# Kernel tuning notes

Measured on AMD Instinct MI355X. Metric: run time of the kernel, lower is better.

Reference implementation:

```python
import jax, jax.numpy as jnp
import numpy as np

B, S, D = 1, 4096, 2048
H, KVH, HD = 16, 4, 128  # heads, kv heads, head_dim
ROPE_BASE = 10000.0


def _rope_cos_sin(position_ids):
    # inv_freq: [HD/2]
    inv_freq = 1.0 / (ROPE_BASE ** (jnp.arange(0, HD, 2, dtype=jnp.float32) / HD))
    # freqs: [B, S, HD/2] -> emb: [B, S, HD] (concat(freqs, freqs))
    freqs = position_ids.astype(jnp.float32)[..., None] * inv_freq
    emb = jnp.concatenate([freqs, freqs], axis=-1)
    # [B, 1, S, HD] to broadcast over heads
    return jnp.cos(emb)[:, None, :, :], jnp.sin(emb)[:, None, :, :]


def _rotate_half(x):
    x1, x2 = x[..., : HD // 2], x[..., HD // 2 :]
    return jnp.concatenate([-x2, x1], axis=-1)


def setup_inputs() -> dict:
    key = jax.random.key(0)
    ks = jax.random.split(key, 5)
    s = 0.02
    return {
        "hidden_states": jax.random.normal(ks[0], (B, S, D), jnp.float32),
        "Wq": jax.random.normal(ks[1], (H * HD, D), jnp.float32) * s,
        "Wk": jax.random.normal(ks[2], (KVH * HD, D), jnp.float32) * s,
        "Wv": jax.random.normal(ks[3], (KVH * HD, D), jnp.float32) * s,
        "Wo": jax.random.normal(ks[4], (D, H * HD), jnp.float32) * s,
        "position_ids": jnp.arange(S, dtype=jnp.int64 if jax.config.jax_enable_x64 else jnp.int32)[None, :].repeat(B, 0),
    }


def reference(hidden_states, Wq, Wk, Wv, Wo, position_ids):
    b, s, _ = hidden_states.shape
    # projections (no bias): [b, s, nheads*hd] -> [b, nh, s, hd]
    q = (hidden_states @ Wq.T).reshape(b, s, H, HD).transpose(0, 2, 1, 3)
    k = (hidden_states @ Wk.T).reshape(b, s, KVH, HD).transpose(0, 2, 1, 3)
    v = (hidden_states @ Wv.T).reshape(b, s, KVH, HD).transpose(0, 2, 1, 3)

    cos, sin = _rope_cos_sin(position_ids)  # [b,1,s,hd]
    q = q * cos + _rotate_half(q) * sin
    k = k * cos + _rotate_half(k) * sin

    # GQA: repeat kv heads (repeat_interleave along head dim)
    n_rep = H // KVH
    k = jnp.repeat(k, n_rep, axis=1)
    v = jnp.repeat(v, n_rep, axis=1)

    # eager quadratic attention with causal mask
    scores = jnp.einsum("bhqd,bhkd->bhqk", q, k) / jnp.sqrt(jnp.float32(HD))
    causal = jnp.tril(jnp.ones((s, s), dtype=bool))
    scores = jnp.where(causal[None, None], scores, jnp.finfo(scores.dtype).min)
    attn = jax.nn.softmax(scores, axis=-1)
    out = jnp.einsum("bhqk,bhkd->bhqd", attn, v)  # [b,h,s,hd]
    out = out.transpose(0, 2, 1, 3).reshape(b, s, H * HD)
    return out @ Wo.T
```

## Files before the change

### kernel.cpp

```cpp
#include <hip/hip_runtime.h>
#include <hip/hip_bf16.h>

constexpr int S   = 4096;
constexpr int D   = 2048;
constexpr int H   = 16;
constexpr int KVH = 4;
constexpr int HD  = 128;

using short8 = __attribute__((ext_vector_type(8))) short;
using f32x4  = __attribute__((ext_vector_type(4))) float;
using f32x16 = __attribute__((ext_vector_type(16))) float;

__device__ inline ushort f2bf(float f) {
  union { float f; unsigned u; } x{f};
  unsigned r = x.u + 0x7FFFu + ((x.u >> 16) & 1u);
  return (ushort)(r >> 16);
}
__device__ inline float bf2f(ushort h) {
  union { unsigned u; float f; } x{(unsigned)h << 16};
  return x.f;
}
__device__ inline unsigned pkbf(float a, float b) {
  union { float f; unsigned u; } xa{a}, xb{b};
  unsigned ra = xa.u + 0x7FFFu + ((xa.u >> 16) & 1u);
  unsigned rb = xb.u + 0x7FFFu + ((xb.u >> 16) & 1u);
#if __has_builtin(__builtin_amdgcn_perm)
  return __builtin_amdgcn_perm(rb, ra, 0x07060302u);
#else
  return (rb & 0xFFFF0000u) | (ra >> 16);
#endif
}
__device__ inline unsigned pkbf_t(float a, float b) {
  union { float f; unsigned u; } xa{a}, xb{b};
#if __has_builtin(__builtin_amdgcn_perm)
  return __builtin_amdgcn_perm(xb.u, xa.u, 0x07060302u);
#else
  return (xb.u & 0xFFFF0000u) | (xa.u >> 16);
#endif
}
__device__ inline float fast_exp2(float x) {
#if __has_builtin(__builtin_amdgcn_exp2f)
  return __builtin_amdgcn_exp2f(x);
#else
  return exp2f(x);
#endif
}

__device__ inline void async_copy16(const ushort* g, ushort* l) {
  __builtin_amdgcn_global_load_lds(
      (const __attribute__((address_space(1))) unsigned int*)g,
      (__attribute__((address_space(3))) unsigned int*)l, 16, 0, 0);
}

constexpr size_t N_HID = (size_t)S * D;
constexpr size_t N_WQ  = (size_t)(H * HD) * D;
constexpr size_t N_WKV = (size_t)(KVH * HD) * D;
constexpr size_t C1_ = N_HID;
constexpr size_t C2_ = C1_ + N_WQ;
constexpr size_t C3_ = C2_ + N_WKV;
constexpr size_t C4_ = C3_ + N_WKV;
constexpr size_t C5_ = C4_ + N_WQ;

__global__ void cvt_all_kernel(const float* __restrict__ hid, const float* __restrict__ wq,
                               const float* __restrict__ wk, const float* __restrict__ wv,
                               const float* __restrict__ wo, ushort* __restrict__ dst) {
  size_t i = (size_t)blockIdx.x * blockDim.x + threadIdx.x;
  size_t off = i * 4;
  if (off >= C5_) return;
  const float* src;
  if      (off < C1_) src = hid + off;
  else if (off < C2_) src = wq + (off - C1_);
  else if (off < C3_) src = wk + (off - C2_);
  else if (off < C4_) src = wv + (off - C3_);
  else                src = wo + (off - C4_);
  float4 f = *(const float4*)src;
  ushort4 o;
  o.x = f2bf(f.x); o.y = f2bf(f.y); o.z = f2bf(f.z); o.w = f2bf(f.w);
  *(ushort4*)&dst[off] = o;
}

template <int OUT_MODE>
__device__ __forceinline__ void gemm_tile(const ushort* __restrict__ A,
                                          const ushort* __restrict__ Bt,
                                          void* __restrict__ Cv,
                                          int M, int N, int K, int bxi, int byi,
                                          ushort* As, ushort* Bs) {
  const int bm = byi * 128;
  const int bn = bxi * 128;
  const int tid  = threadIdx.x;
  const int lane = tid & 63;
  const int w    = tid >> 6;
  const int wr = w >> 1, wc = w & 1;
  const int lm = lane & 15, quad = lane >> 4;

  f32x4 acc[4][4];
#pragma unroll
  for (int i = 0; i < 4; ++i)
#pragma unroll
    for (int j = 0; j < 4; ++j) acc[i][j] = (f32x4){0.f, 0.f, 0.f, 0.f};

  for (int k0 = 0; k0 < K; k0 += 32) {
#pragma unroll
    for (int j = 0; j < 2; ++j) {
      int idx = j * 256 + tid;
      int row = idx >> 2;
      int col = (idx & 3) * 8;
      int ubase = (j * 256 + w * 64) * 8;
      async_copy16(A + (size_t)(bm + row) * K + k0 + col, &As[ubase]);
      async_copy16(Bt + (size_t)(bn + row) * K + k0 + col, &Bs[ubase]);
    }
    __syncthreads();
    short8 af[4], bfr[4];
#pragma unroll
    for (int t = 0; t < 4; ++t) {
      af[t]  = *(const short8*)&As[(wr * 64 + t * 16 + lm) * 32 + quad * 8];
      bfr[t] = *(const short8*)&Bs[(wc * 64 + t * 16 + lm) * 32 + quad * 8];
    }
#pragma unroll
    for (int i = 0; i < 4; ++i)
#pragma unroll
      for (int j = 0; j < 4; ++j)
        acc[i][j] = __builtin_amdgcn_mfma_f32_16x16x32_bf16(af[i], bfr[j], acc[i][j], 0, 0, 0);
    __syncthreads();
  }

#pragma unroll
  for (int i = 0; i < 4; ++i)
#pragma unroll
    for (int j = 0; j < 4; ++j) {
      if (OUT_MODE == 2) {
        int col  = bn + wc * 64 + j * 16 + lm;
        int rowb = bm + wr * 64 + i * 16 + quad * 4;
        ushort4 o4;
        o4.x = f2bf(acc[i][j][0]); o4.y = f2bf(acc[i][j][1]);
        o4.z = f2bf(acc[i][j][2]); o4.w = f2bf(acc[i][j][3]);
        *(ushort4*)&((ushort*)Cv)[(size_t)col * M + rowb] = o4;
      } else {
#pragma unroll
        for (int r = 0; r < 4; ++r) {
          size_t row = bm + wr * 64 + i * 16 + quad * 4 + r;
          size_t col = bn + wc * 64 + j * 16 + lm;
          if (OUT_MODE == 1) ((ushort*)Cv)[row * N + col] = f2bf(acc[i][j][r]);
          else               ((float*)Cv)[row * N + col]  = acc[i][j][r];
        }
      }
    }
}

__global__ __launch_bounds__(256) void gemm_qkv_kernel(const ushort* __restrict__ hb,
                                                       const ushort* __restrict__ wq,
                                                       const ushort* __restrict__ wk,
                                                       const ushort* __restrict__ wv,
                                                       ushort* __restrict__ qb,
                                                       ushort* __restrict__ kb,
                                                       ushort* __restrict__ vtb) {
  __shared__ __align__(16) ushort As[128 * 32];
  __shared__ __align__(16) ushort Bs[128 * 32];
  int bid = blockIdx.x;
  if (bid < 512) {
    gemm_tile<1>(hb, wq, qb, S, H * HD, D, bid & 15, bid >> 4, As, Bs);
  } else if (bid < 640) {
    int b = bid - 512;
    gemm_tile<1>(hb, wk, kb, S, KVH * HD, D, b & 3, b >> 2, As, Bs);
  } else {
    int b = bid - 640;
    gemm_tile<2>(hb, wv, vtb, S, KVH * HD, D, b & 3, b >> 2, As, Bs);
  }
}

template <int OUT_MODE>
__global__ __launch_bounds__(256) void gemm_bt_kernel(const ushort* __restrict__ A,
                                                      const ushort* __restrict__ Bt,
                                                      void* __restrict__ Cv,
                                                      int M, int N, int K) {
  __shared__ __align__(16) ushort As[128 * 32];
  __shared__ __align__(16) ushort Bs[128 * 32];
  gemm_tile<OUT_MODE>(A, Bt, Cv, M, N, K, blockIdx.x, blockIdx.y, As, Bs);
}

__global__ void rope_bf16_kernel(ushort* __restrict__ qb, ushort* __restrict__ kb,
                                 const int* __restrict__ pos_ids) {
  int idx = blockIdx.x * blockDim.x + threadIdx.x;
  const int total = S * (H + KVH) * (HD / 2);
  if (idx >= total) return;
  int j = idx & 63;
  int t = idx >> 6;
  int head = t % (H + KVH);
  int s = t / (H + KVH);
  float p = (float)pos_ids[s];
  float inv_freq = exp2f(-(float)j * (13.287712379549449f / 64.0f));
  float ang = p * inv_freq;
  float c = cosf(ang), sn = sinf(ang);
  ushort* base = (head < H) ? (qb + (size_t)s * (H * HD) + head * HD)
                            : (kb + (size_t)s * (KVH * HD) + (head - H) * HD);
  float x1 = bf2f(base[j]), x2 = bf2f(base[j + 64]);
  base[j]      = f2bf(x1 * c - x2 * sn);
  base[j + 64] = f2bf(x2 * c + x1 * sn);
}

__global__ __launch_bounds__(256, 2) void attn_mfma_kernel(const ushort* __restrict__ q,
                                                           const ushort* __restrict__ k,
                                                           const ushort* __restrict__ Vt,
                                                           ushort* __restrict__ o) {
  const int bid = blockIdx.x;
  const int h   = bid & 15;
  const int t   = bid >> 4;
  const int tl  = t & 15, hi = t >> 4;
  const int qi  = hi ? (2 * tl) : (31 - 2 * tl);
  const int q0  = qi * 128;
  const int kvh = h >> 2;
  const int tid  = threadIdx.x;
  const int lane = tid & 63;
  const int w    = tid >> 6;
  const int m32  = lane & 31;
  const int p    = lane >> 5;

  __shared__ __align__(16) ushort Kc[2][8192];
  __shared__ __align__(16) ushort Vs[2][8192];

  const int q0w = q0 + w * 32;

  short8 qf[8];
#pragma unroll
  for (int s = 0; s < 8; ++s)
    qf[s] = *(const short8*)&q[(size_t)(q0w + m32) * (H * HD) + h * HD + s * 16 + p * 8];

  f32x16 Oacc[4];
#pragma unroll
  for (int i = 0; i < 4; ++i)
#pragma unroll
    for (int r = 0; r < 16; ++r) Oacc[i][r] = 0.f;
  float lsum = 0.f;

  auto stage = [&](int k0, int buf) {
#pragma unroll
    for (int i = 0; i < 8; ++i) {
      int c = w * 8 + i;
      if (c < 16) {
        int kh = c >> 3, s = c & 7;
        async_copy16(&k[(size_t)(k0 + kh * 32 + m32) * (KVH * HD) + kvh * HD + s * 16 + p * 8],
                     &Kc[buf][c * 512]);
      } else {
        int cv = c - 16;
        int ht = cv >> 2, t2 = cv & 3;
        async_copy16(&Vt[(size_t)(kvh * HD + ht * 32 + m32) * S + k0 + t2 * 16 + p * 8],
                     &Vs[buf][cv * 512]);
      }
    }
  };

  stage(0, 0);
  __syncthreads();

  const float C1  = 0.08838834764831845f * 1.4426950408889634f;
  const float F2n = -12.0f * 1.4426950408889634f;
  const int T = 2 * qi + 2;

  for (int tt = 0; tt < T; ++tt) {
    const int k0  = tt * 64;
    const int cur = tt & 1;
    if (tt + 1 < T) stage(k0 + 64, cur ^ 1);
    const ushort* Kb = Kc[cur];
    const ushort* Vb = Vs[cur];

#pragma unroll
    for (int kh = 0; kh < 2; ++kh) {
      const int kbase = k0 + kh * 32;
      if (kbase <= q0w + 31) {
        f32x16 stA, stB;
#pragma unroll
        for (int r = 0; r < 16; ++r) { stA[r] = 0.f; stB[r] = 0.f; }
#pragma unroll
        for (int s = 0; s < 8; s += 2) {
          short8 kf0 = *(const short8*)&Kb[(kh * 8 + s) * 512 + lane * 8];
          short8 kf1 = *(const short8*)&Kb[(kh * 8 + s + 1) * 512 + lane * 8];
          stA = __builtin_amdgcn_mfma_f32_32x32x16_bf16(kf0, qf[s], stA, 0, 0, 0);
          stB = __builtin_amdgcn_mfma_f32_32x32x16_bf16(kf1, qf[s + 1], stB, 0, 0, 0);
        }

        float pv[16];
        if (kbase == q0w) {
#pragma unroll
          for (int r = 0; r < 16; ++r) {
            int kvl = (r & 3) + 8 * (r >> 2) + 4 * p;
            float e = fast_exp2(fmaf(stA[r] + stB[r], C1, F2n));
            e = (kvl > m32) ? 0.f : e;
            pv[r] = e; lsum += e;
          }
        } else {
#pragma unroll
          for (int r = 0; r < 16; ++r) {
            float e = fast_exp2(fmaf(stA[r] + stB[r], C1, F2n));
            pv[r] = e; lsum += e;
          }
        }

        unsigned own2[4][2], oth[4][2];
#pragma unroll
        for (int g = 0; g < 4; ++g) {
          own2[g][0] = pkbf_t(pv[4 * g + 0], pv[4 * g + 1]);
          own2[g][1] = pkbf_t(pv[4 * g + 2], pv[4 * g + 3]);
          oth[g][0]  = __shfl_xor(own2[g][0], 32);
          oth[g][1]  = __shfl_xor(own2[g][1], 32);
        }
        short8 pf[2];
#pragma unroll
        for (int t2 = 0; t2 < 2; ++t2) {
          union { unsigned u4[4]; short8 s8; } pb;
          pb.u4[0] = p ? oth[2 * t2 + 1][0] : own2[2 * t2][0];
          pb.u4[1] = p ? oth[2 * t2 + 1][1] : own2[2 * t2][1];
          pb.u4[2] = p ? own2[2 * t2 + 1][0] : oth[2 * t2][0];
          pb.u4[3] = p ? own2[2 * t2 + 1][1] : oth[2 * t2][1];
          pf[t2] = pb.s8;
        }

#pragma unroll
        for (int ht = 0; ht < 4; ++ht)
#pragma unroll
          for (int t2l = 0; t2l < 2; ++t2l) {
            int cv = ht * 4 + kh * 2 + t2l;
            short8 vf = *(const short8*)&Vb[cv * 512 + lane * 8];
            Oacc[ht] = __builtin_amdgcn_mfma_f32_32x32x16_bf16(vf, pf[t2l], Oacc[ht], 0, 0, 0);
          }
      }
    }
    __syncthreads();
  }

  float ltot = lsum + __shfl_xor(lsum, 32);
  float inv = 1.0f / ltot;
#pragma unroll
  for (int ht = 0; ht < 4; ++ht)
#pragma unroll
    for (int rq = 0; rq < 4; ++rq) {
      uint2 dd;
      dd.x = pkbf(Oacc[ht][4 * rq + 0] * inv, Oacc[ht][4 * rq + 1] * inv);
      dd.y = pkbf(Oacc[ht][4 * rq + 2] * inv, Oacc[ht][4 * rq + 3] * inv);
      *(uint2*)&o[(size_t)(q0w + m32) * (H * HD) + h * HD + ht * 32 + 8 * rq + 4 * p] = dd;
    }
}

extern "C" void kernel_launch(void* const* d_in, const int* in_sizes, int n_in,
                              void* d_out, int out_size, void* d_ws, size_t ws_size,
                              hipStream_t stream) {
  const float* hidden = (const float*)d_in[0];
  const float* Wq     = (const float*)d_in[1];
  const float* Wk     = (const float*)d_in[2];
  const float* Wv     = (const float*)d_in[3];
  const float* Wo     = (const float*)d_in[4];
  const int*   pos    = (const int*)d_in[5];
  float* out = (float*)d_out;

  ushort* hb  = (ushort*)d_ws;
  ushort* wqb = hb  + N_HID;
  ushort* wkb = wqb + N_WQ;
  ushort* wvb = wkb + N_WKV;
  ushort* wob = wvb + N_WKV;
  ushort* qb  = wob + N_WQ;
  ushort* kb  = qb  + (size_t)S * (H * HD);
  ushort* vtb = kb  + (size_t)S * (KVH * HD);
  ushort* ob  = vtb + (size_t)(KVH * HD) * S;

  dim3 blk(256);
  size_t n4 = C5_ / 4;
  cvt_all_kernel<<<(int)((n4 + 255) / 256), blk, 0, stream>>>(hidden, Wq, Wk, Wv, Wo, hb);

  gemm_qkv_kernel<<<dim3(768), blk, 0, stream>>>(hb, wqb, wkb, wvb, qb, kb, vtb);

  int rope_total = S * (H + KVH) * (HD / 2);
  rope_bf16_kernel<<<(rope_total + 255) / 256, blk, 0, stream>>>(qb, kb, pos);

  attn_mfma_kernel<<<dim3(512), blk, 0, stream>>>(qb, kb, vtb, ob);

  gemm_bt_kernel<0><<<dim3(D / 128, S / 128), blk, 0, stream>>>(ob, wob, out, S, D, D);
}
```

Measured before the change: 355.6 us.

## Split attention KV tiles across wave pairs with LDS reduction of partial outputs

The attention block grows from 256 to 512 threads. Each pair of waves now shares a 32-row query slice, with each wave handling one 32-key half of every 64-key tile. Partial row sums and O accumulators are then combined through LDS at the end. Block ordering also changes from interleaved heavy and light query tiles to plain descending order. The aim is more waves per block to hide MFMA and exp latency, at the cost of an extra LDS reduction, more barriers, and possibly lower occupancy from the larger block.

```diff
diff --git a/kernel.cpp b/kernel.cpp
--- a/kernel.cpp
+++ b/kernel.cpp
@@ -198,27 +198,27 @@
   base[j + 64] = f2bf(x2 * c + x1 * sn);
 }
 
-__global__ __launch_bounds__(256, 2) void attn_mfma_kernel(const ushort* __restrict__ q,
-                                                           const ushort* __restrict__ k,
-                                                           const ushort* __restrict__ Vt,
-                                                           ushort* __restrict__ o) {
+__global__ __launch_bounds__(512) void attn_mfma_kernel(const ushort* __restrict__ q,
+                                                        const ushort* __restrict__ k,
+                                                        const ushort* __restrict__ Vt,
+                                                        ushort* __restrict__ o) {
   const int bid = blockIdx.x;
   const int h   = bid & 15;
   const int t   = bid >> 4;
-  const int tl  = t & 15, hi = t >> 4;
-  const int qi  = hi ? (2 * tl) : (31 - 2 * tl);
+  const int qi  = 31 - t;
   const int q0  = qi * 128;
   const int kvh = h >> 2;
   const int tid  = threadIdx.x;
   const int lane = tid & 63;
   const int w    = tid >> 6;
+  const int qw   = w >> 1;
+  const int ks   = w & 1;
   const int m32  = lane & 31;
   const int p    = lane >> 5;
 
-  __shared__ __align__(16) ushort Kc[2][8192];
-  __shared__ __align__(16) ushort Vs[2][8192];
-
-  const int q0w = q0 + w * 32;
+  __shared__ __align__(16) ushort LDSu[32768];
+
+  const int q0w = q0 + qw * 32;
 
   short8 qf[8];
 #pragma unroll
@@ -230,21 +230,21 @@
   for (int i = 0; i < 4; ++i)
 #pragma unroll
     for (int r = 0; r < 16; ++r) Oacc[i][r] = 0.f;
-  float lsum = 0.f;
-
-  auto stage = [&](int k0, int buf) {
-#pragma unroll
-    for (int i = 0; i < 8; ++i) {
-      int c = w * 8 + i;
+  float ls4[4] = {0.f, 0.f, 0.f, 0.f};
+
+  auto stage = [&](int k0s, int buf) {
+#pragma unroll
+    for (int i = 0; i < 4; ++i) {
+      int c = w * 4 + i;
       if (c < 16) {
         int kh = c >> 3, s = c & 7;
-        async_copy16(&k[(size_t)(k0 + kh * 32 + m32) * (KVH * HD) + kvh * HD + s * 16 + p * 8],
-                     &Kc[buf][c * 512]);
+        async_copy16(&k[(size_t)(k0s + kh * 32 + m32) * (KVH * HD) + kvh * HD + s * 16 + p * 8],
+                     &LDSu[buf * 8192 + c * 512]);
       } else {
         int cv = c - 16;
         int ht = cv >> 2, t2 = cv & 3;
-        async_copy16(&Vt[(size_t)(kvh * HD + ht * 32 + m32) * S + k0 + t2 * 16 + p * 8],
-                     &Vs[buf][cv * 512]);
+        async_copy16(&Vt[(size_t)(kvh * HD + ht * 32 + m32) * S + k0s + t2 * 16 + p * 8],
+                     &LDSu[16384 + buf * 8192 + cv * 512]);
       }
     }
   };
@@ -260,84 +260,108 @@
     const int k0  = tt * 64;
     const int cur = tt & 1;
     if (tt + 1 < T) stage(k0 + 64, cur ^ 1);
-    const ushort* Kb = Kc[cur];
-    const ushort* Vb = Vs[cur];
-
-#pragma unroll
-    for (int kh = 0; kh < 2; ++kh) {
-      const int kbase = k0 + kh * 32;
-      if (kbase <= q0w + 31) {
-        f32x16 stA, stB;
-#pragma unroll
-        for (int r = 0; r < 16; ++r) { stA[r] = 0.f; stB[r] = 0.f; }
-#pragma unroll
-        for (int s = 0; s < 8; s += 2) {
-          short8 kf0 = *(const short8*)&Kb[(kh * 8 + s) * 512 + lane * 8];
-          short8 kf1 = *(const short8*)&Kb[(kh * 8 + s + 1) * 512 + lane * 8];
-          stA = __builtin_amdgcn_mfma_f32_32x32x16_bf16(kf0, qf[s], stA, 0, 0, 0);
-          stB = __builtin_amdgcn_mfma_f32_32x32x16_bf16(kf1, qf[s + 1], stB, 0, 0, 0);
+    const ushort* Kb = &LDSu[cur * 8192];
+    const ushort* Vb = &LDSu[16384 + cur * 8192];
+
+    const int kbase = k0 + ks * 32;
+    if (kbase <= q0w + 31) {
+      f32x16 stA, stB;
+#pragma unroll
+      for (int r = 0; r < 16; ++r) { stA[r] = 0.f; stB[r] = 0.f; }
+#pragma unroll
+      for (int s = 0; s < 8; s += 2) {
+        short8 kf0 = *(const short8*)&Kb[(ks * 8 + s) * 512 + lane * 8];
+        short8 kf1 = *(const short8*)&Kb[(ks * 8 + s + 1) * 512 + lane * 8];
+        stA = __builtin_amdgcn_mfma_f32_32x32x16_bf16(kf0, qf[s], stA, 0, 0, 0);
+        stB = __builtin_amdgcn_mfma_f32_32x32x16_bf16(kf1, qf[s + 1], stB, 0, 0, 0);
+      }
+
+      float pv[16];
+      if (kbase == q0w) {
+#pragma unroll
+        for (int r = 0; r < 16; ++r) {
+          int kvl = (r & 3) + 8 * (r >> 2) + 4 * p;
+          float e = fast_exp2(fmaf(stA[r] + stB[r], C1, F2n));
+          e = (kvl > m32) ? 0.f : e;
+          pv[r] = e; ls4[r & 3] += e;
         }
-
-        float pv[16];
-        if (kbase == q0w) {
-#pragma unroll
-          for (int r = 0; r < 16; ++r) {
-            int kvl = (r & 3) + 8 * (r >> 2) + 4 * p;
-            float e = fast_exp2(fmaf(stA[r] + stB[r], C1, F2n));
-            e = (kvl > m32) ? 0.f : e;
-            pv[r] = e; lsum += e;
-          }
-        } else {
-#pragma unroll
-          for (int r = 0; r < 16; ++r) {
-            float e = fast_exp2(fmaf(stA[r] + stB[r], C1, F2n));
-            pv[r] = e; lsum += e;
-          }
+      } else {
+#pragma unroll
+        for (int r = 0; r < 16; ++r) {
+          float e = fast_exp2(fmaf(stA[r] + stB[r], C1, F2n));
+          pv[r] = e; ls4[r & 3] += e;
         }
-
-        unsigned own2[4][2], oth[4][2];
-#pragma unroll
-        for (int g = 0; g < 4; ++g) {
-          own2[g][0] = pkbf_t(pv[4 * g + 0], pv[4 * g + 1]);
-          own2[g][1] = pkbf_t(pv[4 * g + 2], pv[4 * g + 3]);
-          oth[g][0]  = __shfl_xor(own2[g][0], 32);
-          oth[g][1]  = __shfl_xor(own2[g][1], 32);
+      }
+
+      unsigned own2[4][2], oth[4][2];
+#pragma unroll
+      for (int g = 0; g < 4; ++g) {
+        own2[g][0] = pkbf_t(pv[4 * g + 0], pv[4 * g + 1]);
+        own2[g][1] = pkbf_t(pv[4 * g + 2], pv[4 * g + 3]);
+        oth[g][0]  = __shfl_xor(own2[g][0], 32);
+        oth[g][1]  = __shfl_xor(own2[g][1], 32);
+      }
+      short8 pf[2];
+#pragma unroll
+      for (int t2 = 0; t2 < 2; ++t2) {
+        union { unsigned u4[4]; short8 s8; } pb;
+        pb.u4[0] = p ? oth[2 * t2 + 1][0] : own2[2 * t2][0];
+        pb.u4[1] = p ? oth[2 * t2 + 1][1] : own2[2 * t2][1];
+        pb.u4[2] = p ? own2[2 * t2 + 1][0] : oth[2 * t2][0];
+        pb.u4[3] = p ? own2[2 * t2 + 1][1] : oth[2 * t2][1];
+        pf[t2] = pb.s8;
+      }
+
+#pragma unroll
+      for (int ht = 0; ht < 4; ++ht)
+#pragma unroll
+        for (int t2l = 0; t2l < 2; ++t2l) {
+          int cv = ht * 4 + ks * 2 + t2l;
+          short8 vf = *(const short8*)&Vb[cv * 512 + lane * 8];
+          Oacc[ht] = __builtin_amdgcn_mfma_f32_32x32x16_bf16(vf, pf[t2l], Oacc[ht], 0, 0, 0);
         }
-        short8 pf[2];
-#pragma unroll
-        for (int t2 = 0; t2 < 2; ++t2) {
-          union { unsigned u4[4]; short8 s8; } pb;
-          pb.u4[0] = p ? oth[2 * t2 + 1][0] : own2[2 * t2][0];
-          pb.u4[1] = p ? oth[2 * t2 + 1][1] : own2[2 * t2][1];
-          pb.u4[2] = p ? own2[2 * t2 + 1][0] : oth[2 * t2][0];
-          pb.u4[3] = p ? own2[2 * t2 + 1][1] : oth[2 * t2][1];
-          pf[t2] = pb.s8;
-        }
-
-#pragma unroll
-        for (int ht = 0; ht < 4; ++ht)
-#pragma unroll
-          for (int t2l = 0; t2l < 2; ++t2l) {
-            int cv = ht * 4 + kh * 2 + t2l;
-            short8 vf = *(const short8*)&Vb[cv * 512 + lane * 8];
-            Oacc[ht] = __builtin_amdgcn_mfma_f32_32x32x16_bf16(vf, pf[t2l], Oacc[ht], 0, 0, 0);
-          }
-      }
     }
     __syncthreads();
   }
 
-  float ltot = lsum + __shfl_xor(lsum, 32);
-  float inv = 1.0f / ltot;
-#pragma unroll
-  for (int ht = 0; ht < 4; ++ht)
-#pragma unroll
-    for (int rq = 0; rq < 4; ++rq) {
-      uint2 dd;
-      dd.x = pkbf(Oacc[ht][4 * rq + 0] * inv, Oacc[ht][4 * rq + 1] * inv);
-      dd.y = pkbf(Oacc[ht][4 * rq + 2] * inv, Oacc[ht][4 * rq + 3] * inv);
-      *(uint2*)&o[(size_t)(q0w + m32) * (H * HD) + h * HD + ht * 32 + 8 * rq + 4 * p] = dd;
-    }
+  float lsum = (ls4[0] + ls4[1]) + (ls4[2] + ls4[3]);
+  float* mb = (float*)LDSu;
+
+  if (ks) mb[(qw << 6) | lane] = lsum;
+  __syncthreads();
+  if (!ks) lsum += mb[(qw << 6) | lane];
+  __syncthreads();
+
+  if (ks) {
+    float* base = mb + qw * 4096;
+#pragma unroll
+    for (int ht = 0; ht < 4; ++ht)
+#pragma unroll
+      for (int r = 0; r < 16; ++r)
+        base[ht * 1024 + r * 64 + lane] = Oacc[ht][r];
+  }
+  __syncthreads();
+
+  if (!ks) {
+    const float* base = mb + qw * 4096;
+#pragma unroll
+    for (int ht = 0; ht < 4; ++ht)
+#pragma unroll
+      for (int r = 0; r < 16; ++r)
+        Oacc[ht][r] += base[ht * 1024 + r * 64 + lane];
+
+    float ltot = lsum + __shfl_xor(lsum, 32);
+    float inv = 1.0f / ltot;
+#pragma unroll
+    for (int ht = 0; ht < 4; ++ht)
+#pragma unroll
+      for (int rq = 0; rq < 4; ++rq) {
+        uint2 dd;
+        dd.x = pkbf(Oacc[ht][4 * rq + 0] * inv, Oacc[ht][4 * rq + 1] * inv);
+        dd.y = pkbf(Oacc[ht][4 * rq + 2] * inv, Oacc[ht][4 * rq + 3] * inv);
+        *(uint2*)&o[(size_t)(q0w + m32) * (H * HD) + h * HD + ht * 32 + 8 * rq + 4 * p] = dd;
+      }
+  }
 }
 
 extern "C" void kernel_launch(void* const* d_in, const int* in_sizes, int n_in,
@@ -370,7 +394,7 @@
   int rope_total = S * (H + KVH) * (HD / 2);
   rope_bf16_kernel<<<(rope_total + 255) / 256, blk, 0, stream>>>(qb, kb, pos);
 
-  attn_mfma_kernel<<<dim3(512), blk, 0, stream>>>(qb, kb, vtb, ob);
+  attn_mfma_kernel<<<dim3(512), dim3(512), 0, stream>>>(qb, kb, vtb, ob);
 
   gemm_bt_kernel<0><<<dim3(D / 128, S / 128), blk, 0, stream>>>(ob, wob, out, S, D, D);
 }
```

Result: faster. 348.1 us (-2.1%).
